# Performance work log

Hardware: AMD Instinct MI355X
Metric: run time of the kernel (lower is better)

The kernel has to match this reference:

```python
import jax, jax.numpy as jnp
import numpy as np

NUM_HEADS = 8
VALUE_HEAD_DIM = 32
BLOCK_SIZE = 8
SELECT_TOPK = 16
EMBED_DIM = 256
VALUE_DIM = NUM_HEADS * VALUE_HEAD_DIM  # 256


def setup_inputs() -> dict:
    key = jax.random.key(0)
    ks = jax.random.split(key, 8)
    B, H, W = 8, 128, 128
    nbt = (H // BLOCK_SIZE) * (W // BLOCK_SIZE)  # 256
    bs2 = BLOCK_SIZE * BLOCK_SIZE  # 64
    x = jax.random.normal(ks[0], (B, H, W, EMBED_DIM), dtype=jnp.float32)
    # attn weights: normalized over last axis (module expects sum(-1)==1)
    aw = jax.random.uniform(ks[1], (NUM_HEADS, B, nbt, bs2, bs2 + SELECT_TOPK), dtype=jnp.float32)
    attn_weights = aw / jnp.sum(aw, axis=-1, keepdims=True)
    indexes = jax.random.randint(ks[2], (B, nbt, SELECT_TOPK), 0, H * W, dtype=jnp.int32)
    weights = jax.random.uniform(ks[3], (B, nbt, SELECT_TOPK), dtype=jnp.float32)
    W_in = jax.random.normal(ks[4], (EMBED_DIM, VALUE_DIM), dtype=jnp.float32) / np.sqrt(EMBED_DIM)
    b_in = jnp.zeros((VALUE_DIM,), dtype=jnp.float32)
    W_out = 0.05 * jax.random.normal(ks[5], (VALUE_DIM, EMBED_DIM), dtype=jnp.float32) / np.sqrt(VALUE_DIM)
    b_out = jnp.zeros((EMBED_DIM,), dtype=jnp.float32)
    return {"x": x, "attn_weights": attn_weights, "indexes": indexes, "weights": weights,
            "W_in": W_in, "b_in": b_in, "W_out": W_out, "b_out": b_out}


def reference(x, attn_weights, indexes, weights, W_in, b_in, W_out, b_out):
    B, H, W, _ = x.shape
    bs = BLOCK_SIZE
    nbh, nbw = H // bs, W // bs
    nbt = nbh * nbw
    nt = H * W
    nh, vhd, vd, topk = NUM_HEADS, VALUE_HEAD_DIM, VALUE_DIM, SELECT_TOPK

    xp = x @ W_in + b_in  # (B, H, W, vd)
    flat = xp.reshape(B, nt, vd)
    # gather top-k selected tokens per block: (B, nbt, topk, vd)
    sel = jnp.take_along_axis(flat, indexes.reshape(B, nbt * topk, 1), axis=1)
    sel = sel.reshape(B, nbt, topk, vd) * weights[..., None]
    sel = sel.reshape(B, nbt, topk, nh, vhd).transpose(3, 0, 1, 2, 4)  # (nh,B,nbt,topk,vhd)

    # local block values: (nh, B, nbt, bs^2, vhd)
    xb = xp.reshape(B, nbh, bs, nbw, bs, nh, vhd)
    xb = xb.transpose(5, 0, 1, 3, 2, 4, 6).reshape(nh, B, nbt, bs * bs, vhd)
    xb = jnp.concatenate([xb, sel], axis=3)  # (nh,B,nbt,bs^2+topk,vhd)

    out = jnp.matmul(attn_weights, xb)  # (nh,B,nbt,bs^2,vhd)
    out = out.reshape(nh, B, nbh, nbw, bs, bs, vhd)
    out = out.transpose(1, 2, 4, 3, 5, 0, 6).reshape(B, H, W, vd)
    return out @ W_out + b_out
```

## Files before the change

kernel.cpp:

```cpp
#include <hip/hip_runtime.h>


typedef __attribute__((ext_vector_type(4))) float   f32x4;
typedef __attribute__((ext_vector_type(8))) __bf16  bf16x8;
typedef __attribute__((ext_vector_type(4))) __bf16  bf16x4;

#define XPT_STRIDE 160
#define REG_SIZE   5120
#define REG_STRIDE 80
#define LDS_BYTES  40960

__global__ void prep_weights_k(const float* __restrict__ Wi,
                               const float* __restrict__ Wo,
                               __bf16* __restrict__ WiT,
                               __bf16* __restrict__ WoT) {
    int n = blockIdx.x;
    int k = threadIdx.x;
    WiT[n * 256 + k] = (__bf16)Wi[k * 256 + n];
    WoT[n * 256 + k] = (__bf16)Wo[k * 256 + n];
}

__device__ __forceinline__ bf16x8 cvt8(f32x4 lo, f32x4 hi) {
    bf16x8 r;
    r[0] = (__bf16)lo.x; r[1] = (__bf16)lo.y; r[2] = (__bf16)lo.z; r[3] = (__bf16)lo.w;
    r[4] = (__bf16)hi.x; r[5] = (__bf16)hi.y; r[6] = (__bf16)hi.z; r[7] = (__bf16)hi.w;
    return r;
}

__global__
__attribute__((amdgpu_flat_work_group_size(256, 256), amdgpu_waves_per_eu(1, 4)))
void fused_attn_k(
    const float* __restrict__ x,
    const float* __restrict__ aw,
    const int*   __restrict__ idx,
    const float* __restrict__ wts,
    const float* __restrict__ b_in,
    const float* __restrict__ b_out,
    const __bf16* __restrict__ WiT,
    const __bf16* __restrict__ WoT,
    float* __restrict__ out)
{
    __shared__ __align__(16) unsigned char lds[LDS_BYTES];

    const int tid  = threadIdx.x;
    const int lane = tid & 63;
    const int wv   = tid >> 6;
    const int l16  = lane & 15;
    const int q    = lane >> 4;
    const int bid  = blockIdx.x;
    const int b    = bid >> 8;
    const int blk  = bid & 255;
    const int bh   = blk >> 4, bw = blk & 15;
    const int nbase = wv * 64;

    const float* xb   = x   + (size_t)b * 16384 * 256;
    const int*   idxb = idx + (b * 256 + blk) * 16;
    const float* wtsb = wts + (b * 256 + blk) * 16;

    for (int mt = 0; mt < 5; ++mt) {
        int m = mt * 16 + l16;
        int tokA;
        if (m < 64) {
            tokA = ((bh << 3) + (m >> 3)) * 128 + (bw << 3) + (m & 7);
        } else {
            tokA = idxb[m - 64];
        }
        const float* xrow = xb + (size_t)tokA * 256;
        bf16x8 af[8];
        #pragma unroll
        for (int kc = 0; kc < 8; ++kc) {
            const f32x4* p = (const f32x4*)(xrow + kc * 32 + q * 8);
            af[kc] = cvt8(p[0], p[1]);
        }
        float rs[4];
        #pragma unroll
        for (int r = 0; r < 4; ++r) {
            int me = mt * 16 + q * 4 + r;
            rs[r] = (me >= 64) ? wtsb[me - 64] : 1.0f;
        }
        const int j0w = mt * 16 + q * 4;
        #pragma unroll
        for (int n4 = 0; n4 < 4; ++n4) {
            int c = nbase + n4 * 16 + l16;
            f32x4 acc = {0.f, 0.f, 0.f, 0.f};
            const __bf16* wcol = WiT + c * 256 + q * 8;
            #pragma unroll
            for (int kc = 0; kc < 8; ++kc) {
                bf16x8 bfrag = *(const bf16x8*)(wcol + kc * 32);
                acc = __builtin_amdgcn_mfma_f32_16x16x32_bf16(af[kc], bfrag, acc, 0, 0, 0);
            }
            float bias = b_in[c];
            bf16x4 w4;
            #pragma unroll
            for (int r = 0; r < 4; ++r)
                w4[r] = (__bf16)((acc[r] + bias) * rs[r]);
            *(bf16x4*)(lds + c * XPT_STRIDE + j0w * 2) = w4;
        }
    }

    #pragma unroll
    for (int hh = 0; hh < 2; ++hh) {
        const int h = wv * 2 + hh;
        const float* awh = aw + ((size_t)(h * 8 + b) * 256 + blk) * (64 * 80);
        const float* awl = awh + l16 * 80;
        f32x4 acc[2][4];
        #pragma unroll
        for (int md = 0; md < 2; ++md)
            #pragma unroll
            for (int n4 = 0; n4 < 4; ++n4)
                acc[md][n4] = (f32x4){0.f, 0.f, 0.f, 0.f};

        bf16x8 pbf[4];
        #pragma unroll
        for (int n4 = 0; n4 < 4; ++n4) {
            const f32x4* p = (const f32x4*)(awl + n4 * (16 * 80) + q * 8);
            pbf[n4] = cvt8(p[0], p[1]);
        }

        #pragma unroll
        for (int kc = 0; kc < 3; ++kc) {
            f32x4 nb[4][2];
            if (kc < 2) {
                int j0n = (kc + 1) * 32 + q * 8;
                int j0c = (j0n < 80) ? j0n : 0;
                #pragma unroll
                for (int n4 = 0; n4 < 4; ++n4) {
                    const f32x4* p = (const f32x4*)(awl + n4 * (16 * 80) + j0c);
                    nb[n4][0] = p[0]; nb[n4][1] = p[1];
                }
            }
            int j0  = kc * 32 + q * 8;
            int j0a = (j0 < 80) ? j0 : 0;
            bf16x8 a0 = *(const bf16x8*)(lds + (h * 32 + l16) * XPT_STRIDE + j0a * 2);
            bf16x8 a1 = *(const bf16x8*)(lds + (h * 32 + 16 + l16) * XPT_STRIDE + j0a * 2);
            if (j0 >= 80) {
                bf16x8 z = {};
                a0 = z; a1 = z;
            }
            #pragma unroll
            for (int n4 = 0; n4 < 4; ++n4) {
                acc[0][n4] = __builtin_amdgcn_mfma_f32_16x16x32_bf16(a0, pbf[n4], acc[0][n4], 0, 0, 0);
                acc[1][n4] = __builtin_amdgcn_mfma_f32_16x16x32_bf16(a1, pbf[n4], acc[1][n4], 0, 0, 0);
            }
            if (kc < 2) {
                #pragma unroll
                for (int n4 = 0; n4 < 4; ++n4)
                    pbf[n4] = cvt8(nb[n4][0], nb[n4][1]);
            }
        }

        #pragma unroll
        for (int n4 = 0; n4 < 4; ++n4) {
            int i = n4 * 16 + l16;
            #pragma unroll
            for (int md = 0; md < 2; ++md) {
                bf16x4 w4;
                #pragma unroll
                for (int r = 0; r < 4; ++r)
                    w4[r] = (__bf16)acc[md][n4][r];
                int d0 = md * 16 + q * 4;
                *(bf16x4*)(lds + h * REG_SIZE + i * REG_STRIDE + d0 * 2) = w4;
            }
        }
    }

    __syncthreads();

    #pragma unroll
    for (int mt = 0; mt < 4; ++mt) {
        bf16x8 af[8];
        #pragma unroll
        for (int kc = 0; kc < 8; ++kc)
            af[kc] = *(const bf16x8*)(lds + kc * REG_SIZE +
                                      (mt * 16 + l16) * REG_STRIDE + q * 16);
        #pragma unroll
        for (int n4 = 0; n4 < 4; ++n4) {
            int e = nbase + n4 * 16 + l16;
            f32x4 acc = {0.f, 0.f, 0.f, 0.f};
            const __bf16* wcol = WoT + e * 256 + q * 8;
            #pragma unroll
            for (int kc = 0; kc < 8; ++kc) {
                bf16x8 bfrag = *(const bf16x8*)(wcol + kc * 32);
                acc = __builtin_amdgcn_mfma_f32_16x16x32_bf16(af[kc], bfrag, acc, 0, 0, 0);
            }
            float bias = b_out[e];
            #pragma unroll
            for (int r = 0; r < 4; ++r) {
                int ie  = mt * 16 + q * 4 + r;
                int tok = ((bh << 3) + (ie >> 3)) * 128 + (bw << 3) + (ie & 7);
                out[((size_t)b * 16384 + tok) * 256 + e] = acc[r] + bias;
            }
        }
    }
}

extern "C" void kernel_launch(void* const* d_in, const int* in_sizes, int n_in,
                              void* d_out, int out_size, void* d_ws, size_t ws_size,
                              hipStream_t stream) {
    (void)in_sizes; (void)n_in; (void)out_size; (void)ws_size;
    const float* x   = (const float*)d_in[0];
    const float* aw  = (const float*)d_in[1];
    const int*   idx = (const int*)d_in[2];
    const float* wts = (const float*)d_in[3];
    const float* Wi  = (const float*)d_in[4];
    const float* bi  = (const float*)d_in[5];
    const float* Wo  = (const float*)d_in[6];
    const float* bo  = (const float*)d_in[7];

    __bf16* WiT = (__bf16*)d_ws;
    __bf16* WoT = WiT + 256 * 256;
    float*  o   = (float*)d_out;

    prep_weights_k<<<dim3(256), dim3(256), 0, stream>>>(Wi, Wo, WiT, WoT);
    fused_attn_k<<<dim3(2048), dim3(256), 0, stream>>>(
        x, aw, idx, wts, bi, bo, WiT, WoT, o);
}
```

Measured before the change: 753.6 us.

## Stage gathered x rows in swizzled LDS and reuse weight fragments across row tiles

The input projection now loads each gathered x row once, cooperatively, converts it to bf16 and stores it in a swizzled LDS buffer, processed in two parts of 48 and 32 rows. Before, each lane read x straight from global memory in fragment order. Both projections swap loop order so each wave loads a weight column's B fragments once and reuses them across all row tiles, instead of reloading them per tile. LDS use grows to 64KB and the waves-per-EU hint is lowered, which cuts occupancy and adds extra barriers.

```diff
diff --git a/kernel.cpp b/kernel.cpp
--- a/kernel.cpp
+++ b/kernel.cpp
@@ -5,10 +5,12 @@
 typedef __attribute__((ext_vector_type(8))) __bf16  bf16x8;
 typedef __attribute__((ext_vector_type(4))) __bf16  bf16x4;
 
+#define XB_STRIDE  512
+#define XPT_BASE   24576
 #define XPT_STRIDE 160
 #define REG_SIZE   5120
 #define REG_STRIDE 80
-#define LDS_BYTES  40960
+#define LDS_BYTES  65536
 
 __global__ void prep_weights_k(const float* __restrict__ Wi,
                                const float* __restrict__ Wo,
@@ -27,8 +29,35 @@
     return r;
 }
 
+__device__ __forceinline__ void loadb8(bf16x8 (&bf)[8], const __bf16* base) {
+    #pragma unroll
+    for (int kc = 0; kc < 8; ++kc)
+        bf[kc] = *(const bf16x8*)(base + kc * 32);
+}
+
+__device__ __forceinline__ void stage_xb(unsigned char* lds, const float* xb,
+                                         const int* __restrict__ idxb,
+                                         int tid, int bh, int bw,
+                                         int r0, int nr) {
+    for (int rr = 0; rr < (nr >> 4); ++rr) {
+        int j  = r0 + rr * 16 + (tid >> 4);
+        int jl = j - r0;
+        int tokA = (j < 64)
+            ? (((bh << 3) + (j >> 3)) * 128 + (bw << 3) + (j & 7))
+            : idxb[j - 64];
+        const f32x4* v = (const f32x4*)(xb + (size_t)tokA * 256 + (tid & 15) * 16);
+        f32x4 v0 = v[0], v1 = v[1], v2 = v[2], v3 = v[3];
+        bf16x8 w0 = cvt8(v0, v1), w1 = cvt8(v2, v3);
+        int inner = (tid & 15) * 32;
+        int sw = (jl & 7) << 4;
+        unsigned char* base = lds + jl * XB_STRIDE;
+        *(bf16x8*)(base + (inner ^ sw))        = w0;
+        *(bf16x8*)(base + ((inner + 16) ^ sw)) = w1;
+    }
+}
+
 __global__
-__attribute__((amdgpu_flat_work_group_size(256, 256), amdgpu_waves_per_eu(1, 4)))
+__attribute__((amdgpu_flat_work_group_size(256, 256), amdgpu_waves_per_eu(1, 2)))
 void fused_attn_k(
     const float* __restrict__ x,
     const float* __restrict__ aw,
@@ -57,45 +86,53 @@
     const int*   idxb = idx + (b * 256 + blk) * 16;
     const float* wtsb = wts + (b * 256 + blk) * 16;
 
-    for (int mt = 0; mt < 5; ++mt) {
-        int m = mt * 16 + l16;
-        int tokA;
-        if (m < 64) {
-            tokA = ((bh << 3) + (m >> 3)) * 128 + (bw << 3) + (m & 7);
-        } else {
-            tokA = idxb[m - 64];
-        }
-        const float* xrow = xb + (size_t)tokA * 256;
-        bf16x8 af[8];
-        #pragma unroll
-        for (int kc = 0; kc < 8; ++kc) {
-            const f32x4* p = (const f32x4*)(xrow + kc * 32 + q * 8);
-            af[kc] = cvt8(p[0], p[1]);
-        }
-        float rs[4];
-        #pragma unroll
-        for (int r = 0; r < 4; ++r) {
-            int me = mt * 16 + q * 4 + r;
-            rs[r] = (me >= 64) ? wtsb[me - 64] : 1.0f;
-        }
-        const int j0w = mt * 16 + q * 4;
-        #pragma unroll
+    float bi4[4];
+    #pragma unroll
+    for (int n4 = 0; n4 < 4; ++n4)
+        bi4[n4] = b_in[nbase + n4 * 16 + l16];
+
+    for (int part = 0; part < 2; ++part) {
+        const int r0  = part ? 48 : 0;
+        const int nr  = part ? 32 : 48;
+        const int mt0 = part ? 3 : 0;
+        const int mtN = part ? 5 : 3;
+
+        stage_xb(lds, xb, idxb, tid, bh, bw, r0, nr);
+        __syncthreads();
+
         for (int n4 = 0; n4 < 4; ++n4) {
-            int c = nbase + n4 * 16 + l16;
-            f32x4 acc = {0.f, 0.f, 0.f, 0.f};
-            const __bf16* wcol = WiT + c * 256 + q * 8;
-            #pragma unroll
-            for (int kc = 0; kc < 8; ++kc) {
-                bf16x8 bfrag = *(const bf16x8*)(wcol + kc * 32);
-                acc = __builtin_amdgcn_mfma_f32_16x16x32_bf16(af[kc], bfrag, acc, 0, 0, 0);
-            }
-            float bias = b_in[c];
-            bf16x4 w4;
-            #pragma unroll
-            for (int r = 0; r < 4; ++r)
-                w4[r] = (__bf16)((acc[r] + bias) * rs[r]);
-            *(bf16x4*)(lds + c * XPT_STRIDE + j0w * 2) = w4;
-        }
+            const __bf16* wq = WiT + (nbase + n4 * 16 + l16) * 256 + q * 8;
+            bf16x8 bb[8];
+            loadb8(bb, wq);
+            const int c = nbase + n4 * 16 + l16;
+
+            for (int mt = mt0; mt < mtN; ++mt) {
+                int ml = mt * 16 + l16 - r0;
+                int sw = (ml & 7) << 4;
+                bf16x8 af[8];
+                #pragma unroll
+                for (int kc = 0; kc < 8; ++kc)
+                    af[kc] = *(const bf16x8*)(lds + ml * XB_STRIDE +
+                                              ((kc * 64 + q * 16) ^ sw));
+                f32x4 acc = {0.f, 0.f, 0.f, 0.f};
+                #pragma unroll
+                for (int kc = 0; kc < 8; ++kc)
+                    acc = __builtin_amdgcn_mfma_f32_16x16x32_bf16(af[kc], bb[kc], acc, 0, 0, 0);
+                float rs[4];
+                #pragma unroll
+                for (int r = 0; r < 4; ++r) {
+                    int me = mt * 16 + q * 4 + r;
+                    rs[r] = (me >= 64) ? wtsb[me - 64] : 1.0f;
+                }
+                int j0w = mt * 16 + q * 4;
+                bf16x4 w4;
+                #pragma unroll
+                for (int r = 0; r < 4; ++r)
+                    w4[r] = (__bf16)((acc[r] + bi4[n4]) * rs[r]);
+                *(bf16x4*)(lds + XPT_BASE + c * XPT_STRIDE + j0w * 2) = w4;
+            }
+        }
+        if (part == 0) __syncthreads();
     }
 
     #pragma unroll
@@ -131,8 +168,8 @@
             }
             int j0  = kc * 32 + q * 8;
             int j0a = (j0 < 80) ? j0 : 0;
-            bf16x8 a0 = *(const bf16x8*)(lds + (h * 32 + l16) * XPT_STRIDE + j0a * 2);
-            bf16x8 a1 = *(const bf16x8*)(lds + (h * 32 + 16 + l16) * XPT_STRIDE + j0a * 2);
+            bf16x8 a0 = *(const bf16x8*)(lds + XPT_BASE + (h * 32 + l16) * XPT_STRIDE + j0a * 2);
+            bf16x8 a1 = *(const bf16x8*)(lds + XPT_BASE + (h * 32 + 16 + l16) * XPT_STRIDE + j0a * 2);
             if (j0 >= 80) {
                 bf16x8 z = {};
                 a0 = z; a1 = z;
@@ -159,7 +196,7 @@
                 for (int r = 0; r < 4; ++r)
                     w4[r] = (__bf16)acc[md][n4][r];
                 int d0 = md * 16 + q * 4;
-                *(bf16x4*)(lds + h * REG_SIZE + i * REG_STRIDE + d0 * 2) = w4;
+                *(bf16x4*)(lds + XPT_BASE + h * REG_SIZE + i * REG_STRIDE + d0 * 2) = w4;
             }
         }
     }
@@ -167,28 +204,29 @@
     __syncthreads();
 
     #pragma unroll
-    for (int mt = 0; mt < 4; ++mt) {
-        bf16x8 af[8];
-        #pragma unroll
-        for (int kc = 0; kc < 8; ++kc)
-            af[kc] = *(const bf16x8*)(lds + kc * REG_SIZE +
-                                      (mt * 16 + l16) * REG_STRIDE + q * 16);
-        #pragma unroll
-        for (int n4 = 0; n4 < 4; ++n4) {
-            int e = nbase + n4 * 16 + l16;
+    for (int n4 = 0; n4 < 4; ++n4) {
+        const int e = nbase + n4 * 16 + l16;
+        const __bf16* wq = WoT + e * 256 + q * 8;
+        bf16x8 bb[8];
+        loadb8(bb, wq);
+        const float bo = b_out[e];
+
+        #pragma unroll
+        for (int mt = 0; mt < 4; ++mt) {
+            bf16x8 af[8];
+            #pragma unroll
+            for (int kc = 0; kc < 8; ++kc)
+                af[kc] = *(const bf16x8*)(lds + XPT_BASE + kc * REG_SIZE +
+                                          (mt * 16 + l16) * REG_STRIDE + q * 16);
             f32x4 acc = {0.f, 0.f, 0.f, 0.f};
-            const __bf16* wcol = WoT + e * 256 + q * 8;
-            #pragma unroll
-            for (int kc = 0; kc < 8; ++kc) {
-                bf16x8 bfrag = *(const bf16x8*)(wcol + kc * 32);
-                acc = __builtin_amdgcn_mfma_f32_16x16x32_bf16(af[kc], bfrag, acc, 0, 0, 0);
-            }
-            float bias = b_out[e];
+            #pragma unroll
+            for (int kc = 0; kc < 8; ++kc)
+                acc = __builtin_amdgcn_mfma_f32_16x16x32_bf16(af[kc], bb[kc], acc, 0, 0, 0);
             #pragma unroll
             for (int r = 0; r < 4; ++r) {
                 int ie  = mt * 16 + q * 4 + r;
                 int tok = ((bh << 3) + (ie >> 3)) * 128 + (bw << 3) + (ie & 7);
-                out[((size_t)b * 16384 + tok) * 256 + e] = acc[r] + bias;
+                out[((size_t)b * 16384 + tok) * 256 + e] = acc[r] + bo;
             }
         }
     }
```

Result: faster. 614.8 us (-18.4%).
